# Kernel optimization log

Measured on AMD Instinct MI355X. Metric: run time of the kernel, lower is better.

The kernel has to match this reference:

```python
import jax, jax.numpy as jnp
import numpy as np

B, C, D = 256, 50000, 512
ALPHA = 0.5


def setup_inputs() -> dict:
    key = jax.random.key(0)
    k1, k2, k3 = jax.random.split(key, 3)
    x = jax.random.normal(k1, (B, D), dtype=jnp.float32)
    labels = jax.random.randint(k2, (B,), 0, C)
    onehot = jax.nn.one_hot(labels, C, dtype=jnp.float32)  # [B, C]
    # 'uniform' keras initializer -> U(-0.05, 0.05)
    centers = jax.random.uniform(k3, (C, D), dtype=jnp.float32, minval=-0.05, maxval=0.05)
    return {"x": x, "onehot": onehot, "centers": centers}


def reference(x, onehot, centers):
    # gather-as-matmul: selected center per sample, [B, D]
    sel = jnp.matmul(onehot, centers)
    # scatter-add-as-matmul: per-class accumulated delta, [C, D]
    delta_centers = jnp.matmul(onehot.T, sel - x)
    # per-class counts (+1), [C, 1]
    center_counts = jnp.sum(onehot.T, axis=1, keepdims=True) + 1.0
    delta_centers = delta_centers / center_counts
    new_centers = centers - ALPHA * delta_centers
    # squared distance to (old) center, [B, 1]
    diff = x - sel
    result = jnp.sum(diff * diff, axis=1, keepdims=True)
    return result, new_centers
```

## Files before the change

### kernel.cpp

```cpp
#include <hip/hip_runtime.h>

#define B_N 256
#define C_N 50000
#define D_N 512
#define ALPHA 0.5f

__global__ __launch_bounds__(256) void find_labels(
        const float* __restrict__ onehot,
        int* __restrict__ labels,
        int* __restrict__ counts) {
    int idx = blockIdx.x * 256 + threadIdx.x;
    const int total4 = B_N * C_N / 4;
    if (idx >= total4) return;
    const float4* p = (const float4*)onehot;
    float4 v = p[idx];
    if (v.x != 0.f || v.y != 0.f || v.z != 0.f || v.w != 0.f) {
        int base = idx * 4;
        float f[4] = {v.x, v.y, v.z, v.w};
#pragma unroll
        for (int k = 0; k < 4; ++k) {
            if (f[k] != 0.f) {
                int g = base + k;
                int b = g / C_N;
                int c = g - b * C_N;
                labels[b] = c;
                atomicAdd(&counts[c], 1);
            }
        }
    }
}

__global__ __launch_bounds__(128) void sq_dist(
        const float* __restrict__ x,
        const float* __restrict__ centers,
        const int* __restrict__ labels,
        float* __restrict__ result) {
    int b = blockIdx.x;
    int t = threadIdx.x;
    int lab = labels[b];
    float4 xv = ((const float4*)(x + (size_t)b * D_N))[t];
    float4 cv = ((const float4*)(centers + (size_t)lab * D_N))[t];
    float dx = xv.x - cv.x, dy = xv.y - cv.y, dz = xv.z - cv.z, dw = xv.w - cv.w;
    float s = dx * dx + dy * dy + dz * dz + dw * dw;
#pragma unroll
    for (int off = 32; off > 0; off >>= 1) s += __shfl_down(s, off, 64);
    __shared__ float ws[2];
    if ((t & 63) == 0) ws[t >> 6] = s;
    __syncthreads();
    if (t == 0) result[b] = ws[0] + ws[1];
}

__global__ __launch_bounds__(128) void update_centers(
        const float* __restrict__ x,
        const float* __restrict__ centers,
        const int* __restrict__ labels,
        const int* __restrict__ counts,
        float* __restrict__ newc) {
    int c = blockIdx.x;
    int t = threadIdx.x;
    int n = counts[c];
    float4 cv = ((const float4*)(centers + (size_t)c * D_N))[t];
    float4 res;
    if (n == 0) {
        res = cv;
    } else {
        float4 sx = make_float4(0.f, 0.f, 0.f, 0.f);
        for (int b = 0; b < B_N; ++b) {
            if (labels[b] == c) {
                float4 xv = ((const float4*)(x + (size_t)b * D_N))[t];
                sx.x += xv.x; sx.y += xv.y; sx.z += xv.z; sx.w += xv.w;
            }
        }
        float inv = 1.0f / (float)(n + 1);
        float ac = 1.0f - ALPHA * (float)n * inv;
        float bc = ALPHA * inv;
        res.x = cv.x * ac + sx.x * bc;
        res.y = cv.y * ac + sx.y * bc;
        res.z = cv.z * ac + sx.z * bc;
        res.w = cv.w * ac + sx.w * bc;
    }
    ((float4*)(newc + (size_t)c * D_N))[t] = res;
}

extern "C" void kernel_launch(void* const* d_in, const int* in_sizes, int n_in,
                              void* d_out, int out_size, void* d_ws, size_t ws_size,
                              hipStream_t stream) {
    const float* x       = (const float*)d_in[0];
    const float* onehot  = (const float*)d_in[1];
    const float* centers = (const float*)d_in[2];
    float* out    = (float*)d_out;
    float* result = out;
    float* newc   = out + B_N;

    int* counts = (int*)d_ws;
    int* labels = counts + C_N;

    hipMemsetAsync(counts, 0, C_N * sizeof(int), stream);

    const int total4 = B_N * C_N / 4;
    find_labels<<<(total4 + 255) / 256, 256, 0, stream>>>(onehot, labels, counts);
    sq_dist<<<B_N, 128, 0, stream>>>(x, centers, labels, result);
    update_centers<<<C_N, 128, 0, stream>>>(x, centers, labels, counts, newc);
}
```

Baseline: 226.8 us.

## Fuse onehot scan with center copy, update only touched classes

Merges the onehot label scan with a bulk streaming copy of centers into new_centers in one grid-stride kernel that uses nontemporal loads and stores. A second kernel computes the squared distances and rewrites only the centers of classes that appear in the batch. The first block per class does the write and computes the count itself, so the counts memset and atomics go away. This removes the 50000-block update kernel that read every center and scanned the labels per class. The touched-class rows are overwritten after the copy, which relies on ordering between the two kernels.

```diff
diff --git a/kernel.cpp b/kernel.cpp
--- a/kernel.cpp
+++ b/kernel.cpp
@@ -5,81 +5,86 @@
 #define D_N 512
 #define ALPHA 0.5f
 
-__global__ __launch_bounds__(256) void find_labels(
+typedef float v4f __attribute__((ext_vector_type(4)));
+
+#define ONEHOT4 (B_N * (C_N / 4))
+#define CENT4   (C_N * (D_N / 4))
+#define TOTAL4  (ONEHOT4 + CENT4)
+
+__global__ __launch_bounds__(256) void scan_copy(
         const float* __restrict__ onehot,
-        int* __restrict__ labels,
-        int* __restrict__ counts) {
-    int idx = blockIdx.x * 256 + threadIdx.x;
-    const int total4 = B_N * C_N / 4;
-    if (idx >= total4) return;
-    const float4* p = (const float4*)onehot;
-    float4 v = p[idx];
-    if (v.x != 0.f || v.y != 0.f || v.z != 0.f || v.w != 0.f) {
-        int base = idx * 4;
-        float f[4] = {v.x, v.y, v.z, v.w};
+        const v4f* __restrict__ centers4,
+        v4f* __restrict__ newc4,
+        int* __restrict__ labels) {
+    const v4f* oh4 = (const v4f*)onehot;
+    const int stride = gridDim.x * 256;
+    for (int i = blockIdx.x * 256 + threadIdx.x; i < TOTAL4; i += stride) {
+        if (i < ONEHOT4) {
+            v4f v = __builtin_nontemporal_load(oh4 + i);
+            if (v[0] != 0.f || v[1] != 0.f || v[2] != 0.f || v[3] != 0.f) {
+                int base = i * 4;
 #pragma unroll
-        for (int k = 0; k < 4; ++k) {
-            if (f[k] != 0.f) {
-                int g = base + k;
-                int b = g / C_N;
-                int c = g - b * C_N;
-                labels[b] = c;
-                atomicAdd(&counts[c], 1);
+                for (int k = 0; k < 4; ++k) {
+                    if (v[k] != 0.f) {
+                        int g = base + k;
+                        int b = g / C_N;
+                        labels[b] = g - b * C_N;
+                    }
+                }
             }
+        } else {
+            int j = i - ONEHOT4;
+            __builtin_nontemporal_store(__builtin_nontemporal_load(centers4 + j),
+                                        newc4 + j);
         }
     }
 }
 
-__global__ __launch_bounds__(128) void sq_dist(
+__global__ __launch_bounds__(128) void finish(
         const float* __restrict__ x,
         const float* __restrict__ centers,
         const int* __restrict__ labels,
-        float* __restrict__ result) {
-    int b = blockIdx.x;
+        float* __restrict__ result,
+        float* __restrict__ newc) {
+    __shared__ int lab[B_N];
+    __shared__ float ws[2];
     int t = threadIdx.x;
-    int lab = labels[b];
-    float4 xv = ((const float4*)(x + (size_t)b * D_N))[t];
-    float4 cv = ((const float4*)(centers + (size_t)lab * D_N))[t];
-    float dx = xv.x - cv.x, dy = xv.y - cv.y, dz = xv.z - cv.z, dw = xv.w - cv.w;
-    float s = dx * dx + dy * dy + dz * dz + dw * dw;
+    lab[t] = labels[t];
+    lab[t + 128] = labels[t + 128];
+    __syncthreads();
+
+    if (blockIdx.x < B_N) {
+        int b = blockIdx.x;
+        int c = lab[b];
+        v4f xv = ((const v4f*)(x + (size_t)b * D_N))[t];
+        v4f cv = ((const v4f*)(centers + (size_t)c * D_N))[t];
+        v4f d = xv - cv;
+        float s = d[0] * d[0] + d[1] * d[1] + d[2] * d[2] + d[3] * d[3];
 #pragma unroll
-    for (int off = 32; off > 0; off >>= 1) s += __shfl_down(s, off, 64);
-    __shared__ float ws[2];
-    if ((t & 63) == 0) ws[t >> 6] = s;
-    __syncthreads();
-    if (t == 0) result[b] = ws[0] + ws[1];
-}
-
-__global__ __launch_bounds__(128) void update_centers(
-        const float* __restrict__ x,
-        const float* __restrict__ centers,
-        const int* __restrict__ labels,
-        const int* __restrict__ counts,
-        float* __restrict__ newc) {
-    int c = blockIdx.x;
-    int t = threadIdx.x;
-    int n = counts[c];
-    float4 cv = ((const float4*)(centers + (size_t)c * D_N))[t];
-    float4 res;
-    if (n == 0) {
-        res = cv;
+        for (int off = 32; off > 0; off >>= 1) s += __shfl_down(s, off, 64);
+        if ((t & 63) == 0) ws[t >> 6] = s;
+        __syncthreads();
+        if (t == 0) result[b] = ws[0] + ws[1];
     } else {
-        float4 sx = make_float4(0.f, 0.f, 0.f, 0.f);
-        for (int b = 0; b < B_N; ++b) {
-            if (labels[b] == c) {
-                float4 xv = ((const float4*)(x + (size_t)b * D_N))[t];
-                sx.x += xv.x; sx.y += xv.y; sx.z += xv.z; sx.w += xv.w;
+        int b = blockIdx.x - B_N;
+        int c = lab[b];
+        for (int i = 0; i < b; ++i)
+            if (lab[i] == c) return;
+        int n = 0;
+        v4f sx = {0.f, 0.f, 0.f, 0.f};
+        for (int i = 0; i < B_N; ++i) {
+            if (lab[i] == c) {
+                ++n;
+                sx += ((const v4f*)(x + (size_t)i * D_N))[t];
             }
         }
         float inv = 1.0f / (float)(n + 1);
         float ac = 1.0f - ALPHA * (float)n * inv;
         float bc = ALPHA * inv;
-        res.x = cv.x * ac + sx.x * bc;
-        res.y = cv.y * ac + sx.y * bc;
-        res.z = cv.z * ac + sx.z * bc;
-        res.w = cv.w * ac + sx.w * bc;
+        v4f cv = ((const v4f*)(centers + (size_t)c * D_N))[t];
+        v4f res = cv * ac + sx * bc;
+        ((v4f*)(newc + (size_t)c * D_N))[t] = res;
     }
-    ((float4*)(newc + (size_t)c * D_N))[t] = res;
 }
 
 extern "C" void kernel_launch(void* const* d_in, const int* in_sizes, int n_in,
@@ -92,13 +97,9 @@
     float* result = out;
     float* newc   = out + B_N;
 
-    int* counts = (int*)d_ws;
-    int* labels = counts + C_N;
+    int* labels = (int*)d_ws;
 
-    hipMemsetAsync(counts, 0, C_N * sizeof(int), stream);
-
-    const int total4 = B_N * C_N / 4;
-    find_labels<<<(total4 + 255) / 256, 256, 0, stream>>>(onehot, labels, counts);
-    sq_dist<<<B_N, 128, 0, stream>>>(x, centers, labels, result);
-    update_centers<<<C_N, 128, 0, stream>>>(x, centers, labels, counts, newc);
+    scan_copy<<<2048, 256, 0, stream>>>(onehot, (const v4f*)centers,
+                                        (v4f*)newc, labels);
+    finish<<<512, 128, 0, stream>>>(x, centers, labels, result, newc);
 }
```

Result: slower. 240.3 us (+6.0%).
